# Kernel tuning notes

Measured on AMD Instinct MI355X. Metric: run time of the kernel, lower is better.

Reference implementation:

```python
import jax, jax.numpy as jnp
import numpy as np

N = 50000        # nodes
E = 800000       # edges (avg degree 16)
D_IN = 128
D_OUT = 128
P_DROP = 0.1
BN_EPS = 1e-5


def setup_inputs() -> dict:
    key = jax.random.key(0)
    k1, k2, k3 = jax.random.split(key, 3)
    x = jax.random.normal(k1, (N, D_IN), dtype=jnp.float32)
    edge_index = jax.random.randint(k2, (2, E), 0, N, dtype=jnp.int64)
    W = jax.random.normal(k3, (D_IN, D_OUT), dtype=jnp.float32) / np.sqrt(D_IN).astype(np.float32)
    b = jnp.zeros((D_OUT,), jnp.float32)
    bn_gamma = jnp.ones((D_OUT,), jnp.float32)
    bn_beta = jnp.zeros((D_OUT,), jnp.float32)
    return {"x": x, "edge_index": edge_index, "W": W, "b": b,
            "bn_gamma": bn_gamma, "bn_beta": bn_beta}


def reference(x, edge_index, W, b, bn_gamma, bn_beta):
    n = x.shape[0]
    # --- GCNConv: h = x W, symmetric-normalized aggregation with self-loops ---
    h = x @ W                                            # [N, D_OUT]
    loops = jnp.arange(n, dtype=edge_index.dtype)
    src = jnp.concatenate([edge_index[0], loops])        # [E+N]
    dst = jnp.concatenate([edge_index[1], loops])        # [E+N]
    deg = jax.ops.segment_sum(jnp.ones_like(dst, h.dtype), dst, num_segments=n)
    dinv = jax.lax.rsqrt(jnp.maximum(deg, 1.0))          # deg >= 1 (self-loops)
    norm = dinv[src] * dinv[dst]                         # [E+N]
    msg = h[src] * norm[:, None]                         # gather + weight
    z = jax.ops.segment_sum(msg, dst, num_segments=n) + b
    # --- activation ---
    z = jax.nn.relu(z)
    # --- BatchNorm over nodes (training-mode batch statistics) ---
    mean = z.mean(axis=0)
    var = z.var(axis=0)
    z = bn_gamma * (z - mean) * jax.lax.rsqrt(var + BN_EPS) + bn_beta
    # --- dropout (training mode, fixed key for determinism) ---
    keep = jax.random.bernoulli(jax.random.key(42), 1.0 - P_DROP, z.shape)
    z = jnp.where(keep, z / (1.0 - P_DROP), 0.0)
    return z.astype(x.dtype)
```

## Files before the change

### kernel.cpp

```cpp
#include <hip/hip_runtime.h>
#include <stdint.h>


#define NN 50000
#define NE 800000
#define DD 128
#define SCAN_B 256
#define NSB ((NN + SCAN_B - 1) / SCAN_B)
#define NSTAT 400

using f32x4  = __attribute__((ext_vector_type(4))) float;
using short8 = __attribute__((ext_vector_type(8))) short;

__device__ __forceinline__ uint32_t rotl32(uint32_t x, uint32_t d) {
  return (x << d) | (x >> (32u - d));
}

__device__ __forceinline__ uint32_t threefry_bits(uint32_t idx) {
  const uint32_t ks0 = 0u;
  const uint32_t ks1 = 42u;
  const uint32_t ks2 = 0x1BD11BDAu ^ ks0 ^ ks1;
  uint32_t x0 = ks0;
  uint32_t x1 = idx + ks1;
#define TF_R(r) { x0 += x1; x1 = rotl32(x1, (r)); x1 ^= x0; }
  TF_R(13u) TF_R(15u) TF_R(26u) TF_R(6u)
  x0 += ks1; x1 += ks2 + 1u;
  TF_R(17u) TF_R(29u) TF_R(16u) TF_R(24u)
  x0 += ks2; x1 += ks0 + 2u;
  TF_R(13u) TF_R(15u) TF_R(26u) TF_R(6u)
  x0 += ks0; x1 += ks1 + 3u;
  TF_R(17u) TF_R(29u) TF_R(16u) TF_R(24u)
  x0 += ks1; x1 += ks2 + 4u;
  TF_R(13u) TF_R(15u) TF_R(26u) TF_R(6u)
  x0 += ks2; x1 += ks0 + 5u;
#undef TF_R
  return x0 ^ x1;
}

__device__ __forceinline__ uint32_t f2bf(float f) {
  uint32_t u = __float_as_uint(f);
  return (u + 0x7fffu + ((u >> 16) & 1u)) >> 16;
}
__device__ __forceinline__ float bf2f(uint32_t h) { return __uint_as_float(h << 16); }
__device__ __forceinline__ float bf_lo(uint32_t p) { return __uint_as_float(p << 16); }
__device__ __forceinline__ float bf_hi(uint32_t p) { return __uint_as_float(p & 0xffff0000u); }

__global__ __launch_bounds__(256) void k_wpack(const float* __restrict__ Wm,
                                               short8* __restrict__ wfh,
                                               short8* __restrict__ wfl) {
  int tid = blockIdx.x * 256 + threadIdx.x;
  if (tid >= 32 * 64) return;
  int lane = tid & 63;
  int cfks = tid >> 6;
  int ks = cfks >> 3, cf = cfks & 7;
  int krow = ks * 32 + ((lane >> 4) << 3);
  int col = cf * 16 + (lane & 15);
  short8 h, l;
#pragma unroll
  for (int j = 0; j < 8; ++j) {
    float w = Wm[(size_t)(krow + j) * DD + col];
    uint32_t hb = f2bf(w);
    uint32_t lb = f2bf(w - bf2f(hb));
    h[j] = (short)hb;
    l[j] = (short)lb;
  }
  wfh[tid] = h;
  wfl[tid] = l;
}

#define GBM 128
__global__ __launch_bounds__(256) void k_gemm(const float* __restrict__ x,
                                              const short8* __restrict__ wfh,
                                              const short8* __restrict__ wfl,
                                              const float* __restrict__ dinv,
                                              uint16_t* __restrict__ hbf) {
  __shared__ uint4 ldsbuf[4096];
  char* lds = (char*)ldsbuf;
  const int t = threadIdx.x;
  const int row0 = blockIdx.x * GBM;
  const int c4 = t & 31, rbase = t >> 5;

#pragma unroll
  for (int i = 0; i < 16; ++i) {
    int r = rbase + i * 8;
    int grow = row0 + r;
    float4 v = make_float4(0.f, 0.f, 0.f, 0.f);
    if (grow < NN)
      v = *reinterpret_cast<const float4*>(&x[(size_t)grow * DD + c4 * 4]);
    uint32_t h0 = f2bf(v.x), h1 = f2bf(v.y), h2 = f2bf(v.z), h3 = f2bf(v.w);
    uint32_t l0 = f2bf(v.x - bf2f(h0)), l1 = f2bf(v.y - bf2f(h1));
    uint32_t l2 = f2bf(v.z - bf2f(h2)), l3 = f2bf(v.w - bf2f(h3));
    int byte = (r * 256 + c4 * 8) ^ ((r & 7) << 4);
    *reinterpret_cast<uint2*>(lds + byte) = make_uint2(h0 | (h1 << 16), h2 | (h3 << 16));
    *reinterpret_cast<uint2*>(lds + 32768 + byte) = make_uint2(l0 | (l1 << 16), l2 | (l3 << 16));
  }
  __syncthreads();

  const int wv = t >> 6, l = t & 63;
  f32x4 acc[2][8] = {};
#pragma unroll
  for (int ks = 0; ks < 4; ++ks) {
    short8 ah[2], al[2];
#pragma unroll
    for (int rf = 0; rf < 2; ++rf) {
      int r = wv * 32 + rf * 16 + (l & 15);
      int byte = (r * 256 + ks * 64 + ((l >> 4) << 4)) ^ ((r & 7) << 4);
      ah[rf] = *reinterpret_cast<const short8*>(lds + byte);
      al[rf] = *reinterpret_cast<const short8*>(lds + 32768 + byte);
    }
#pragma unroll
    for (int cf = 0; cf < 8; ++cf) {
      short8 bh = wfh[(ks * 8 + cf) * 64 + l];
      short8 bl = wfl[(ks * 8 + cf) * 64 + l];
#pragma unroll
      for (int rf = 0; rf < 2; ++rf) {
        acc[rf][cf] = __builtin_amdgcn_mfma_f32_16x16x32_bf16(ah[rf], bl, acc[rf][cf], 0, 0, 0);
        acc[rf][cf] = __builtin_amdgcn_mfma_f32_16x16x32_bf16(al[rf], bh, acc[rf][cf], 0, 0, 0);
        acc[rf][cf] = __builtin_amdgcn_mfma_f32_16x16x32_bf16(ah[rf], bh, acc[rf][cf], 0, 0, 0);
      }
    }
  }
  __syncthreads();

#pragma unroll
  for (int rf = 0; rf < 2; ++rf)
#pragma unroll
    for (int i = 0; i < 4; ++i) {
      int row = wv * 32 + rf * 16 + ((l >> 4) << 2) + i;
      int grow = row0 + row;
      float dv = (grow < NN) ? dinv[grow] : 0.f;
#pragma unroll
      for (int cf = 0; cf < 8; ++cf) {
        int col = cf * 16 + (l & 15);
        int byte = (row * 256 + col * 2) ^ ((row & 7) << 4);
        *reinterpret_cast<uint16_t*>(lds + byte) = (uint16_t)f2bf(acc[rf][cf][i] * dv);
      }
    }
  __syncthreads();
#pragma unroll
  for (int i = 0; i < 16; ++i) {
    int r = rbase + i * 8;
    int grow = row0 + r;
    if (grow < NN) {
      int byte = (r * 256 + c4 * 8) ^ ((r & 7) << 4);
      uint2 v = *reinterpret_cast<const uint2*>(lds + byte);
      *reinterpret_cast<uint2*>(&hbf[(size_t)grow * DD + c4 * 4]) = v;
    }
  }
}

__global__ void k_count(const int* __restrict__ ei, int* __restrict__ cnt,
                        uint32_t* __restrict__ pos2) {
  int e2 = blockIdx.x * blockDim.x + threadIdx.x;
  int e = e2 * 2;
  if (e < NE) {
    int2 d = *reinterpret_cast<const int2*>(&ei[NE + e]);
    uint32_t p0 = (uint32_t)atomicAdd(&cnt[d.x], 1) & 0xffffu;
    uint32_t p1 = (uint32_t)atomicAdd(&cnt[d.y], 1) & 0xffffu;
    pos2[e2] = p0 | (p1 << 16);
  }
}

__global__ __launch_bounds__(SCAN_B) void k_scan1(const int* __restrict__ cnt,
                                                  int* __restrict__ tmp,
                                                  int* __restrict__ blk_sums,
                                                  float* __restrict__ dinv) {
  __shared__ int sm[SCAN_B];
  int t = threadIdx.x;
  int i = blockIdx.x * SCAN_B + t;
  int v = (i < NN) ? cnt[i] : 0;
  if (i < NN) dinv[i] = rsqrtf((float)v + 1.0f);
  sm[t] = v;
  __syncthreads();
  for (int off = 1; off < SCAN_B; off <<= 1) {
    int u = (t >= off) ? sm[t - off] : 0;
    __syncthreads();
    sm[t] += u;
    __syncthreads();
  }
  if (i < NN) tmp[i] = sm[t];
  if (t == SCAN_B - 1) blk_sums[blockIdx.x] = sm[t];
}

__global__ __launch_bounds__(SCAN_B) void k_scan3(const int* __restrict__ tmp,
                                                  const int* __restrict__ blk_sums,
                                                  int* __restrict__ row_ptr) {
  __shared__ int sm[SCAN_B];
  int t = threadIdx.x;
  int v = (t < NSB) ? blk_sums[t] : 0;
  sm[t] = v;
  __syncthreads();
  for (int off = 1; off < SCAN_B; off <<= 1) {
    int u = (t >= off) ? sm[t - off] : 0;
    __syncthreads();
    sm[t] += u;
    __syncthreads();
  }
  int excl = sm[blockIdx.x] - blk_sums[blockIdx.x];
  int i = blockIdx.x * SCAN_B + t;
  if (i < NN) {
    row_ptr[i + 1] = tmp[i] + excl;
    if (i == 0) row_ptr[0] = 0;
  }
}

__global__ void k_fill(const int* __restrict__ ei, const int* __restrict__ row_ptr,
                       const uint32_t* __restrict__ pos2, uint16_t* __restrict__ colv) {
  int e2 = blockIdx.x * blockDim.x + threadIdx.x;
  int e = e2 * 2;
  if (e < NE) {
    int2 s = *reinterpret_cast<const int2*>(&ei[e]);
    int2 d = *reinterpret_cast<const int2*>(&ei[NE + e]);
    uint32_t pp = pos2[e2];
    colv[row_ptr[d.x] + (int)(pp & 0xffffu)] = (uint16_t)s.x;
    colv[row_ptr[d.y] + (int)(pp >> 16)]     = (uint16_t)s.y;
  }
}

__global__ __launch_bounds__(256) void k_agg(const uint16_t* __restrict__ hbf,
                                             const int* __restrict__ row_ptr,
                                             const uint16_t* __restrict__ colv,
                                             const float* __restrict__ dinv,
                                             const float* __restrict__ bias,
                                             float* __restrict__ z) {
  int wave = threadIdx.x >> 6;
  int lane = threadIdx.x & 63;
  int node = blockIdx.x * 4 + wave;
  if (node >= NN) return;
  const uint32_t* hp = reinterpret_cast<const uint32_t*>(hbf);

  uint32_t ms = hp[(size_t)node * 64 + lane];
  float ax = bf_lo(ms), ay = bf_hi(ms);

  int e = row_ptr[node], end = row_ptr[node + 1];
  while (e + 16 <= end) {
    int s[16]; uint32_t m[16];
#pragma unroll
    for (int q = 0; q < 16; ++q) s[q] = colv[e + q];
#pragma unroll
    for (int q = 0; q < 16; ++q) m[q] = hp[(size_t)s[q] * 64 + lane];
#pragma unroll
    for (int q = 0; q < 16; ++q) {
      ax += bf_lo(m[q]);
      ay += bf_hi(m[q]);
    }
    e += 16;
  }
  while (e + 8 <= end) {
    int s[8]; uint32_t m[8];
#pragma unroll
    for (int q = 0; q < 8; ++q) s[q] = colv[e + q];
#pragma unroll
    for (int q = 0; q < 8; ++q) m[q] = hp[(size_t)s[q] * 64 + lane];
#pragma unroll
    for (int q = 0; q < 8; ++q) {
      ax += bf_lo(m[q]);
      ay += bf_hi(m[q]);
    }
    e += 8;
  }
  while (e < end) {
    uint32_t m0 = hp[(size_t)colv[e] * 64 + lane];
    ax += bf_lo(m0);
    ay += bf_hi(m0);
    ++e;
  }
  float di = dinv[node];
  float2 bb = reinterpret_cast<const float2*>(bias)[lane];
  float zx = fmaxf(fmaf(ax, di, bb.x), 0.f);
  float zy = fmaxf(fmaf(ay, di, bb.y), 0.f);
  reinterpret_cast<float2*>(z)[(size_t)node * 64 + lane] = make_float2(zx, zy);
}

__global__ __launch_bounds__(256) void k_stats(const float* __restrict__ z,
                                               float* __restrict__ part) {
  int t = threadIdx.x;
  int c4 = t & 31;
  int rgrp = t >> 5;
  float sx = 0.f, sy = 0.f, sz = 0.f, sw = 0.f;
  float qx = 0.f, qy = 0.f, qz = 0.f, qw = 0.f;
  for (int r = blockIdx.x * 8 + rgrp; r < NN; r += NSTAT * 8) {
    float4 v = *reinterpret_cast<const float4*>(&z[(size_t)r * DD + c4 * 4]);
    sx += v.x; sy += v.y; sz += v.z; sw += v.w;
    qx = fmaf(v.x, v.x, qx); qy = fmaf(v.y, v.y, qy);
    qz = fmaf(v.z, v.z, qz); qw = fmaf(v.w, v.w, qw);
  }
  __shared__ float sm[2048], sm2[2048];
  sm[t * 4 + 0] = sx; sm[t * 4 + 1] = sy; sm[t * 4 + 2] = sz; sm[t * 4 + 3] = sw;
  sm2[t * 4 + 0] = qx; sm2[t * 4 + 1] = qy; sm2[t * 4 + 2] = qz; sm2[t * 4 + 3] = qw;
  __syncthreads();
  int c = t & 127;
  float acc = 0.f;
  if (t < 128) {
#pragma unroll
    for (int g = 0; g < 8; ++g) acc += sm[g * 128 + c];
  } else {
#pragma unroll
    for (int g = 0; g < 8; ++g) acc += sm2[g * 128 + c];
  }
  part[blockIdx.x * 256 + t] = acc;
}

__global__ __launch_bounds__(256) void k_stats2(const float* __restrict__ part,
                                                float* __restrict__ bn_sum,
                                                float* __restrict__ bn_sumsq) {
  int t = threadIdx.x;
  float acc = 0.f;
  for (int b = 0; b < NSTAT; ++b) acc += part[b * 256 + t];
  if (t < 128) bn_sum[t] = acc;
  else bn_sumsq[t - 128] = acc;
}

__global__ __launch_bounds__(256) void k_final(float* __restrict__ z,
                                               const float* __restrict__ bn_sum,
                                               const float* __restrict__ bn_sumsq,
                                               const float* __restrict__ gamma,
                                               const float* __restrict__ beta) {
  int j4 = blockIdx.x * blockDim.x + threadIdx.x;
  if (j4 >= NN * DD / 4) return;
  int c4 = j4 & 31;
  const float invN = 1.0f / (float)NN;
  float4 s = *reinterpret_cast<const float4*>(&bn_sum[c4 * 4]);
  float4 q = *reinterpret_cast<const float4*>(&bn_sumsq[c4 * 4]);
  float4 g = *reinterpret_cast<const float4*>(&gamma[c4 * 4]);
  float4 bt = *reinterpret_cast<const float4*>(&beta[c4 * 4]);
  float4 v = *reinterpret_cast<const float4*>(&z[(size_t)j4 * 4]);
  float out[4];
  float mm[4] = {s.x * invN, s.y * invN, s.z * invN, s.w * invN};
  float qq[4] = {q.x * invN, q.y * invN, q.z * invN, q.w * invN};
  float gg[4] = {g.x, g.y, g.z, g.w};
  float bb[4] = {bt.x, bt.y, bt.z, bt.w};
  float vv[4] = {v.x, v.y, v.z, v.w};
#pragma unroll
  for (int i = 0; i < 4; ++i) {
    float var = qq[i] - mm[i] * mm[i];
    float rs = rsqrtf(var + 1e-5f);
    float val = (vv[i] - mm[i]) * rs * gg[i] + bb[i];
    uint32_t bits = threefry_bits((uint32_t)(j4 * 4 + i));
    float u = __uint_as_float((bits >> 9) | 0x3f800000u) - 1.0f;
    out[i] = (u < 0.9f) ? val * (1.0f / 0.9f) : 0.0f;
  }
  *reinterpret_cast<float4*>(&z[(size_t)j4 * 4]) = make_float4(out[0], out[1], out[2], out[3]);
}

extern "C" void kernel_launch(void* const* d_in, const int* in_sizes, int n_in,
                              void* d_out, int out_size, void* d_ws, size_t ws_size,
                              hipStream_t stream) {
  const float* x     = (const float*)d_in[0];
  const int*   ei    = (const int*)d_in[1];
  const float* Wm    = (const float*)d_in[2];
  const float* bvec  = (const float*)d_in[3];
  const float* gamma = (const float*)d_in[4];
  const float* beta  = (const float*)d_in[5];
  float* zout = (float*)d_out;

  uint16_t* hbf  = (uint16_t*)d_ws;
  short8* wfh    = (short8*)(hbf + (size_t)NN * DD);
  short8* wfl    = wfh + 2048;
  uint16_t* colv = (uint16_t*)(wfl + 2048);
  uint32_t* pos2 = (uint32_t*)(colv + NE);
  int* cnt       = (int*)(pos2 + NE / 2);
  float* bn_sum  = (float*)(cnt + NN);
  float* bn_sumsq= bn_sum + DD;
  int* tmp_scan  = (int*)(bn_sumsq + DD);
  int* row_ptr   = tmp_scan + NN;
  float* dinv    = (float*)(row_ptr + NN + 1);
  int* blk_sums  = (int*)(dinv + NN);
  float* part    = (float*)(blk_sums + NSB);

  hipMemsetAsync(cnt, 0, (size_t)NN * sizeof(int), stream);

  k_wpack<<<8, 256, 0, stream>>>(Wm, wfh, wfl);
  k_count<<<(NE / 2 + 255) / 256, 256, 0, stream>>>(ei, cnt, pos2);
  k_scan1<<<NSB, SCAN_B, 0, stream>>>(cnt, tmp_scan, blk_sums, dinv);
  k_scan3<<<NSB, SCAN_B, 0, stream>>>(tmp_scan, blk_sums, row_ptr);
  k_gemm<<<(NN + GBM - 1) / GBM, 256, 0, stream>>>(x, wfh, wfl, dinv, hbf);
  k_fill<<<(NE / 2 + 255) / 256, 256, 0, stream>>>(ei, row_ptr, pos2, colv);
  k_agg<<<(NN + 3) / 4, 256, 0, stream>>>(hbf, row_ptr, colv, dinv, bvec, zout);
  k_stats<<<NSTAT, 256, 0, stream>>>(zout, part);
  k_stats2<<<1, 256, 0, stream>>>(part, bn_sum, bn_sumsq);
  k_final<<<(NN * DD / 4 + 255) / 256, 256, 0, stream>>>(zout, bn_sum, bn_sumsq, gamma, beta);
}
```

Before: 160.5 us.

## Store h in column-chunked layout and aggregate per chunk with 4 edges per wave

New measurement: 211.6 us. +31.8%, slower.

```diff
diff --git a/kernel.cpp b/kernel.cpp
--- a/kernel.cpp
+++ b/kernel.cpp
@@ -73,7 +73,7 @@
                                               const short8* __restrict__ wfh,
                                               const short8* __restrict__ wfl,
                                               const float* __restrict__ dinv,
-                                              uint16_t* __restrict__ hbf) {
+                                              uint2* __restrict__ hc2) {
   __shared__ uint4 ldsbuf[4096];
   char* lds = (char*)ldsbuf;
   const int t = threadIdx.x;
@@ -144,7 +144,7 @@
     if (grow < NN) {
       int byte = (r * 256 + c4 * 8) ^ ((r & 7) << 4);
       uint2 v = *reinterpret_cast<const uint2*>(lds + byte);
-      *reinterpret_cast<uint2*>(&hbf[(size_t)grow * DD + c4 * 4]) = v;
+      hc2[(size_t)(c4 >> 3) * NN * 8 + (size_t)grow * 8 + (c4 & 7)] = v;
     }
   }
 }
@@ -217,59 +217,47 @@
   }
 }
 
-__global__ __launch_bounds__(256) void k_agg(const uint16_t* __restrict__ hbf,
+__global__ __launch_bounds__(256) void k_agg(const uint32_t* __restrict__ hc,
                                              const int* __restrict__ row_ptr,
                                              const uint16_t* __restrict__ colv,
                                              const float* __restrict__ dinv,
                                              const float* __restrict__ bias,
                                              float* __restrict__ z) {
+  int bid = blockIdx.x;
   int wave = threadIdx.x >> 6;
   int lane = threadIdx.x & 63;
-  int node = blockIdx.x * 4 + wave;
-  if (node >= NN) return;
-  const uint32_t* hp = reinterpret_cast<const uint32_t*>(hbf);
-
-  uint32_t ms = hp[(size_t)node * 64 + lane];
-  float ax = bf_lo(ms), ay = bf_hi(ms);
-
-  int e = row_ptr[node], end = row_ptr[node + 1];
-  while (e + 16 <= end) {
-    int s[16]; uint32_t m[16];
-#pragma unroll
-    for (int q = 0; q < 16; ++q) s[q] = colv[e + q];
-#pragma unroll
-    for (int q = 0; q < 16; ++q) m[q] = hp[(size_t)s[q] * 64 + lane];
-#pragma unroll
-    for (int q = 0; q < 16; ++q) {
-      ax += bf_lo(m[q]);
-      ay += bf_hi(m[q]);
-    }
-    e += 16;
-  }
-  while (e + 8 <= end) {
-    int s[8]; uint32_t m[8];
-#pragma unroll
-    for (int q = 0; q < 8; ++q) s[q] = colv[e + q];
-#pragma unroll
-    for (int q = 0; q < 8; ++q) m[q] = hp[(size_t)s[q] * 64 + lane];
-#pragma unroll
-    for (int q = 0; q < 8; ++q) {
-      ax += bf_lo(m[q]);
-      ay += bf_hi(m[q]);
-    }
-    e += 8;
-  }
-  while (e < end) {
-    uint32_t m0 = hp[(size_t)colv[e] * 64 + lane];
-    ax += bf_lo(m0);
-    ay += bf_hi(m0);
-    ++e;
-  }
-  float di = dinv[node];
-  float2 bb = reinterpret_cast<const float2*>(bias)[lane];
-  float zx = fmaxf(fmaf(ax, di, bb.x), 0.f);
-  float zy = fmaxf(fmaf(ay, di, bb.y), 0.f);
-  reinterpret_cast<float2*>(z)[(size_t)node * 64 + lane] = make_float2(zx, zy);
+  int sub = bid & 7;
+  int chunk = sub >> 1;
+  int ng = (bid >> 3) * 2 + (sub & 1);
+  int node = ng * 4 + wave;
+  int eg = lane >> 4;
+  int ch2 = lane & 15;
+
+  const uint32_t* hcc = hc + (size_t)chunk * NN * 16;
+  float ax = 0.f, ay = 0.f;
+  int beg = row_ptr[node], end = row_ptr[node + 1];
+  for (int base = beg; base < end; base += 4) {
+    int ee = base + eg;
+    bool ok = ee < end;
+    int s = colv[ok ? ee : beg];
+    uint32_t m = hcc[(size_t)s * 16 + ch2];
+    m = ok ? m : 0u;
+    ax += bf_lo(m);
+    ay += bf_hi(m);
+  }
+  ax += __shfl_xor(ax, 16); ay += __shfl_xor(ay, 16);
+  ax += __shfl_xor(ax, 32); ay += __shfl_xor(ay, 32);
+  if (lane < 16) {
+    uint32_t ms = hcc[(size_t)node * 16 + ch2];
+    ax += bf_lo(ms);
+    ay += bf_hi(ms);
+    float di = dinv[node];
+    int col = chunk * 32 + ch2 * 2;
+    float2 bb = *reinterpret_cast<const float2*>(&bias[col]);
+    float zx = fmaxf(fmaf(ax, di, bb.x), 0.f);
+    float zy = fmaxf(fmaf(ay, di, bb.y), 0.f);
+    *reinterpret_cast<float2*>(&z[(size_t)node * DD + col]) = make_float2(zx, zy);
+  }
 }
 
 __global__ __launch_bounds__(256) void k_stats(const float* __restrict__ z,
@@ -354,8 +342,9 @@
   const float* beta  = (const float*)d_in[5];
   float* zout = (float*)d_out;
 
-  uint16_t* hbf  = (uint16_t*)d_ws;
-  short8* wfh    = (short8*)(hbf + (size_t)NN * DD);
+  uint32_t* hc   = (uint32_t*)d_ws;
+  short8* wfh    = (short8*)(hc + (size_t)NN * 16 * 4 / 4 * 4);
+  wfh            = (short8*)((uint16_t*)d_ws + (size_t)NN * DD);
   short8* wfl    = wfh + 2048;
   uint16_t* colv = (uint16_t*)(wfl + 2048);
   uint32_t* pos2 = (uint32_t*)(colv + NE);
@@ -374,9 +363,9 @@
   k_count<<<(NE / 2 + 255) / 256, 256, 0, stream>>>(ei, cnt, pos2);
   k_scan1<<<NSB, SCAN_B, 0, stream>>>(cnt, tmp_scan, blk_sums, dinv);
   k_scan3<<<NSB, SCAN_B, 0, stream>>>(tmp_scan, blk_sums, row_ptr);
-  k_gemm<<<(NN + GBM - 1) / GBM, 256, 0, stream>>>(x, wfh, wfl, dinv, hbf);
+  k_gemm<<<(NN + GBM - 1) / GBM, 256, 0, stream>>>(x, wfh, wfl, dinv, (uint2*)hc);
   k_fill<<<(NE / 2 + 255) / 256, 256, 0, stream>>>(ei, row_ptr, pos2, colv);
-  k_agg<<<(NN + 3) / 4, 256, 0, stream>>>(hbf, row_ptr, colv, dinv, bvec, zout);
+  k_agg<<<12500 * 4, 256, 0, stream>>>(hc, row_ptr, colv, dinv, bvec, zout);
   k_stats<<<NSTAT, 256, 0, stream>>>(zout, part);
   k_stats2<<<1, 256, 0, stream>>>(part, bn_sum, bn_sumsq);
   k_final<<<(NN * DD / 4 + 255) / 256, 256, 0, stream>>>(zout, bn_sum, bn_sumsq, gamma, beta);
```
